# Kernel tuning notes

Measured on AMD Instinct MI355X. Metric: run time of the kernel, lower is better.

Reference implementation:

```python
import jax, jax.numpy as jnp
import numpy as np

B, T, N, F_IN, F_OUT = 2, 8, 8192, 128, 32

def setup_inputs() -> dict:
    key = jax.random.key(0)
    k1, k2, k3, k4 = jax.random.split(key, 4)
    inp = jax.random.normal(k1, (B, T, N, F_IN), dtype=jnp.float32)
    adj = jax.random.randint(k2, (N, N), 0, 2, dtype=jnp.int32)
    # xavier_uniform with gain=1.414 ~ std = gain*sqrt(2/(fan_in+fan_out)); gaussian approx
    w_std = 1.414 * np.sqrt(2.0 / (F_IN + F_OUT))
    a_std = 1.414 * np.sqrt(2.0 / (2 * F_OUT + N))
    W = jax.random.normal(k3, (F_IN, F_OUT), dtype=jnp.float32) * w_std
    a = jax.random.normal(k4, (2 * F_OUT, N), dtype=jnp.float32) * a_std
    return {"inp": inp, "adj": adj, "W": W, "a": a}

def reference(inp, adj, W, a):
    # h: [B,T,N,out]
    h = jnp.einsum('btni,io->btno', inp, W)
    out = W.shape[1]
    # mask[j,i] = 1 if j is a neighbor of i (original: torch.where(adj[:, i] > 0))
    mask = (adj > 0).astype(h.dtype)
    # neighbor sum per destination node i: [B,T,N,out]
    nbr = jnp.einsum('ji,btjo->btio', mask, h)
    a1 = a[:out].T   # [N, out], per-node first half of attention vector
    a2 = a[out:].T   # [N, out], per-node second half
    # scalar score per (b,t,i); broadcast across j in the original attention matrix.
    # no-neighbor case coincides since nbr is zero there.
    s = jnp.einsum('btno,no->btn', h, a1) + jnp.einsum('btno,no->btn', nbr, a2)
    # h_prime[b,t,i,:] = s[b,t,i] * sum_j h[b,t,j,:]  (attention row is constant)
    h_prime = s[..., None] * jnp.sum(h, axis=2, keepdims=True)
    return jax.nn.relu(h_prime)
```

## Files before the change

### kernel.cpp

```cpp
#include <hip/hip_runtime.h>

#define BT 16
#define NN 8192
#define FIN 128
#define FOUT 32
#define NB 512
#define SPLITK 4
#define KSPAN (NN / SPLITK)
#define BKK 32
#define NT 64
#define PADA 40

typedef __attribute__((ext_vector_type(8))) short short8;
typedef __attribute__((ext_vector_type(4))) float float4v;

__device__ __forceinline__ float bf2f(unsigned short u) {
    unsigned v = ((unsigned)u) << 16;
    float f;
    __builtin_memcpy(&f, &v, 4);
    return f;
}
__device__ __forceinline__ unsigned short f2bf(float f) {
    unsigned u;
    __builtin_memcpy(&u, &f, 4);
    u += 0x7FFFu + ((u >> 16) & 1u);
    return (unsigned short)(u >> 16);
}

__device__ __forceinline__ void load_lds16(const unsigned short* g, unsigned short* l) {
    __builtin_amdgcn_global_load_lds((const __attribute__((address_space(1))) void*)g,
                                     (__attribute__((address_space(3))) void*)l, 16, 0, 0);
}

__global__ void sniff_dtype(const unsigned* __restrict__ Wraw, unsigned* __restrict__ flag,
                            float* __restrict__ sumh) {
    int lane = threadIdx.x;
    unsigned u = Wraw[lane];
    float f = bf2f((unsigned short)(u & 0xFFFFu));
    float af = fabsf(f);
    bool plaus = (af > 1e-5f) && (af < 1e3f);
    unsigned long long msk = __ballot(plaus);
    if (lane == 0) flag[0] = (__popcll(msk) >= 32) ? 1u : 0u;
#pragma unroll
    for (int r = 0; r < 8; ++r) sumh[lane + 64 * r] = 0.f;
}

__launch_bounds__(256)
__global__ void k1(const void* __restrict__ inp_raw, const void* __restrict__ W_raw,
                   unsigned short* __restrict__ Ht, float* __restrict__ sumh,
                   float4* __restrict__ s2v, const unsigned* __restrict__ flagp) {
    __shared__ __align__(16) unsigned short Wt[32 * 136];
    int bid = blockIdx.x;
    const int tid = threadIdx.x;

    if (bid < 128) {
        float4 z; z.x = z.y = z.z = z.w = 0.f;
        s2v[bid * 256 + tid] = z;
        return;
    }
    bid -= 128;
    const int bt = bid >> 6;
    const int j0 = (bid & 63) * 128;
    const bool isbf = (*flagp != 0u);

    if (isbf) {
        const unsigned short* Wb = (const unsigned short*)W_raw;
#pragma unroll
        for (int r = 0; r < 16; ++r) {
            int idx = tid + 256 * r, i = idx >> 5, o = idx & 31;
            Wt[o * 136 + i] = Wb[idx];
        }
    } else {
        const float* Wf = (const float*)W_raw;
#pragma unroll
        for (int r = 0; r < 16; ++r) {
            int idx = tid + 256 * r, i = idx >> 5, o = idx & 31;
            Wt[o * 136 + i] = f2bf(Wf[idx]);
        }
    }
    __syncthreads();

    const int lane = tid & 63, w = tid >> 6;
    const int m = lane & 15, q = lane >> 4;
    const int mt = (w & 1) * 16;
    const int nt = (w >> 1) * 64;

    float4v acc[4];
#pragma unroll
    for (int c = 0; c < 4; ++c) { float4v z = {0.f, 0.f, 0.f, 0.f}; acc[c] = z; }

#pragma unroll
    for (int kstep = 0; kstep < 4; ++kstep) {
        short8 af = *(const short8*)&Wt[(mt + m) * 136 + kstep * 32 + q * 8];
#pragma unroll
        for (int c = 0; c < 4; ++c) {
            int j = j0 + nt + c * 16 + m;
            short8 bfrag;
            if (isbf) {
                bfrag = *(const short8*)((const unsigned short*)inp_raw +
                        ((size_t)bt * NN + j) * FIN + kstep * 32 + q * 8);
            } else {
                const float* fp = (const float*)inp_raw + ((size_t)bt * NN + j) * FIN + kstep * 32 + q * 8;
                float4 f0 = *(const float4*)fp;
                float4 f1 = *(const float4*)(fp + 4);
                union { unsigned short u[8]; short8 v; } t;
                t.u[0] = f2bf(f0.x); t.u[1] = f2bf(f0.y); t.u[2] = f2bf(f0.z); t.u[3] = f2bf(f0.w);
                t.u[4] = f2bf(f1.x); t.u[5] = f2bf(f1.y); t.u[6] = f2bf(f1.z); t.u[7] = f2bf(f1.w);
                bfrag = t.v;
            }
            acc[c] = __builtin_amdgcn_mfma_f32_16x16x32_bf16(af, bfrag, acc[c], 0, 0, 0);
        }
    }

#pragma unroll
    for (int c = 0; c < 4; ++c) {
#pragma unroll
        for (int e = 0; e < 4; ++e) {
            int o = mt + q * 4 + e;
            int j = j0 + nt + c * 16 + m;
            Ht[(size_t)(bt * FOUT + o) * NN + j] = f2bf(acc[c][e]);
        }
    }
#pragma unroll
    for (int e = 0; e < 4; ++e) {
        float s = acc[0][e] + acc[1][e] + acc[2][e] + acc[3][e];
        s += __shfl_xor(s, 1); s += __shfl_xor(s, 2);
        s += __shfl_xor(s, 4); s += __shfl_xor(s, 8);
        if (m == 0) atomicAdd(&sumh[bt * FOUT + mt + q * 4 + e], s);
    }
}

__launch_bounds__(512, 4)
__global__ void k2_fused(const int* __restrict__ adj, const unsigned short* __restrict__ Ht,
                         const void* __restrict__ a_raw, float* __restrict__ s2,
                         const unsigned* __restrict__ flagp) {
    __shared__ int Pl[KSPAN * 2];
    __shared__ __align__(16) unsigned short As[64 * PADA];
    __shared__ __align__(16) unsigned short Bs[512 * 32];
    const int tid = threadIdx.x;
    const int lane = tid & 63;
    const int w = tid >> 6;
    const int m = lane & 15, q = lane >> 4;
    const int wn = w * 64;

    const int bid = blockIdx.x;
    const int xcd = bid & 7;
    const int z = xcd >> 1;
    const int ib = (bid >> 3) | ((xcd & 1) << 6);
    const int i0 = ib * 64;
    const int zbase = z * KSPAN;

    {
        const int* arow = adj + (size_t)zbase * NN + i0 + lane;
        for (int r0 = 0; r0 < 256; r0 += 16) {
            int v[16];
#pragma unroll
            for (int j = 0; j < 16; ++j)
                v[j] = arow[(size_t)(w * 256 + r0 + j) * NN];
#pragma unroll
            for (int j = 0; j < 16; ++j) {
                unsigned long long b = __ballot(v[j] > 0);
                if (lane == 0) {
                    int k = w * 256 + r0 + j;
                    int2 t;
                    t.x = (int)(unsigned)(b & 0xFFFFFFFFull);
                    t.y = (int)(unsigned)(b >> 32);
                    *(int2*)&Pl[k * 2] = t;
                }
            }
        }
    }

    int boff[4];
#pragma unroll
    for (int c = 0; c < 4; ++c) {
        int u = (w * 4 + c) * 64 + lane;
        int kbs = (u & 3) ^ ((u >> 3) & 3);
        boff[c] = (u >> 2) * NN + kbs * 8;
    }

    float4v acc[4][4];
#pragma unroll
    for (int r = 0; r < 4; ++r)
#pragma unroll
        for (int c = 0; c < 4; ++c) { float4v zz = {0.f, 0.f, 0.f, 0.f}; acc[r][c] = zz; }

    __syncthreads();

    for (int t = 0; t < NT; ++t) {
#pragma unroll
        for (int c = 0; c < 4; ++c)
            load_lds16(Ht + boff[c] + zbase + t * BKK, &Bs[(w * 4 + c) * 512]);
        {
            const int kb = t * BKK + w * 4;
            const int h = lane >> 5, sh = lane & 31;
            unsigned w0 = ((unsigned)Pl[(kb + 0) * 2 + h] >> sh) & 1u;
            unsigned w1 = ((unsigned)Pl[(kb + 1) * 2 + h] >> sh) & 1u;
            unsigned w2 = ((unsigned)Pl[(kb + 2) * 2 + h] >> sh) & 1u;
            unsigned w3 = ((unsigned)Pl[(kb + 3) * 2 + h] >> sh) & 1u;
            int2 tt;
            tt.x = (int)((w0 ? 0x3F80u : 0u) | (w1 ? 0x3F800000u : 0u));
            tt.y = (int)((w2 ? 0x3F80u : 0u) | (w3 ? 0x3F800000u : 0u));
            *(int2*)&As[lane * PADA + w * 4] = tt;
        }
        __syncthreads();
        short8 af[4];
#pragma unroll
        for (int r = 0; r < 4; ++r)
            af[r] = *(const short8*)&As[(r * 16 + m) * PADA + q * 8];
#pragma unroll
        for (int c = 0; c < 4; ++c) {
            int row = wn + c * 16 + m;
            int kbs = q ^ ((m >> 1) & 3);
            short8 bfr = *(const short8*)&Bs[row * 32 + kbs * 8];
#pragma unroll
            for (int r = 0; r < 4; ++r)
                acc[r][c] = __builtin_amdgcn_mfma_f32_16x16x32_bf16(af[r], bfr, acc[r][c], 0, 0, 0);
        }
        __syncthreads();
    }

    const bool isbf = (*flagp != 0u);
    const int btA = wn >> 5;
#pragma unroll
    for (int r = 0; r < 4; ++r) {
#pragma unroll
        for (int e = 0; e < 4; ++e) {
            int gi = i0 + r * 16 + q * 4 + e;
            float a2m, a2m16;
            if (isbf) {
                const unsigned short* ab = (const unsigned short*)a_raw;
                a2m   = bf2f(ab[(size_t)(FOUT + m) * NN + gi]);
                a2m16 = bf2f(ab[(size_t)(FOUT + 16 + m) * NN + gi]);
            } else {
                const float* afp = (const float*)a_raw;
                a2m   = afp[(size_t)(FOUT + m) * NN + gi];
                a2m16 = afp[(size_t)(FOUT + 16 + m) * NN + gi];
            }
            float sA = acc[r][0][e] * a2m + acc[r][1][e] * a2m16;
            float sB = acc[r][2][e] * a2m + acc[r][3][e] * a2m16;
            sA += __shfl_xor(sA, 1); sA += __shfl_xor(sA, 2);
            sA += __shfl_xor(sA, 4); sA += __shfl_xor(sA, 8);
            sB += __shfl_xor(sB, 1); sB += __shfl_xor(sB, 2);
            sB += __shfl_xor(sB, 4); sB += __shfl_xor(sB, 8);
            if (m == 0) {
                atomicAdd(&s2[(size_t)btA * NN + gi], sA);
                atomicAdd(&s2[(size_t)(btA + 1) * NN + gi], sB);
            }
        }
    }
}

__launch_bounds__(256)
__global__ void k3_out(const unsigned short* __restrict__ Ht, const float* __restrict__ s2,
                       const float* __restrict__ sumh, const void* __restrict__ a_raw,
                       void* __restrict__ out_raw, const unsigned* __restrict__ flagp) {
    const int i = blockIdx.x * 256 + threadIdx.x;
    const int bt = blockIdx.y;
    const bool isbf = (*flagp != 0u);

    float s = s2[(size_t)bt * NN + i];
    if (isbf) {
        const unsigned short* ab = (const unsigned short*)a_raw;
#pragma unroll
        for (int o = 0; o < 32; ++o) {
            float h = bf2f(Ht[(size_t)(bt * FOUT + o) * NN + i]);
            s += h * bf2f(ab[(size_t)o * NN + i]);
        }
    } else {
        const float* afp = (const float*)a_raw;
#pragma unroll
        for (int o = 0; o < 32; ++o) {
            float h = bf2f(Ht[(size_t)(bt * FOUT + o) * NN + i]);
            s += h * afp[(size_t)o * NN + i];
        }
    }

    float ov[32];
#pragma unroll
    for (int o = 0; o < 32; ++o) ov[o] = fmaxf(s * sumh[bt * FOUT + o], 0.f);

    size_t ob = ((size_t)bt * NN + i) * FOUT;
    if (isbf) {
        unsigned short* o16 = (unsigned short*)out_raw + ob;
#pragma unroll
        for (int c = 0; c < 8; ++c) {
            ushort4 p;
            p.x = f2bf(ov[c * 4 + 0]); p.y = f2bf(ov[c * 4 + 1]);
            p.z = f2bf(ov[c * 4 + 2]); p.w = f2bf(ov[c * 4 + 3]);
            *(ushort4*)(o16 + c * 4) = p;
        }
    } else {
        float* of = (float*)out_raw + ob;
#pragma unroll
        for (int c = 0; c < 8; ++c) {
            float4 v;
            v.x = ov[c * 4 + 0]; v.y = ov[c * 4 + 1]; v.z = ov[c * 4 + 2]; v.w = ov[c * 4 + 3];
            *(float4*)(of + c * 4) = v;
        }
    }
}

extern "C" void kernel_launch(void* const* d_in, const int* in_sizes, int n_in,
                              void* d_out, int out_size, void* d_ws, size_t ws_size,
                              hipStream_t stream) {
    const void* inp = d_in[0];
    const int* adj = (const int*)d_in[1];
    const void* W = d_in[2];
    const void* a = d_in[3];

    char* ws = (char*)d_ws;
    unsigned short* Ht = (unsigned short*)ws;
    unsigned* flag = (unsigned*)(ws + 8388608);
    float* s2 = (float*)(ws + 8388608 + 4096);
    float* sumh = (float*)(ws + 8388608 + 4096 + 524288);

    sniff_dtype<<<1, 64, 0, stream>>>((const unsigned*)W, flag, sumh);
    k1<<<1152, 256, 0, stream>>>(inp, W, Ht, sumh, (float4*)s2, flag);
    k2_fused<<<512, 512, 0, stream>>>(adj, Ht, a, s2, flag);
    k3_out<<<dim3(NN / 256, BT), 256, 0, stream>>>(Ht, s2, sumh, a, d_out, flag);
}
```

Measured before the change: 539.6 us.

## Reassociate neighbor score as H·a2 then masked sum, row-major H layout

The neighbor-aggregation kernel now computes h_j·a2_i for every (j,i) pair with MFMA and then applies the adjacency mask as per-element FMAs. Before, it formed the masked matrix product mask^T·H and dotted the result with a2 afterwards. H is stored row-major ([bt,j,o]) so each node's features load as contiguous vectors in k1, k2 and k3. The k2 tiling changes to 512-wide i tiles, 256-long k spans and 1024-thread blocks that accumulate all 16 bt slices in registers. This removes the bf16 mask-matrix build in LDS and the large accumulator tile, in exchange for many small MFMAs with zero initial accumulators, masked scalar reduction work, and a2 converted to bf16.

```diff
diff --git a/kernel.cpp b/kernel.cpp
--- a/kernel.cpp
+++ b/kernel.cpp
@@ -4,12 +4,9 @@
 #define NN 8192
 #define FIN 128
 #define FOUT 32
-#define NB 512
-#define SPLITK 4
-#define KSPAN (NN / SPLITK)
-#define BKK 32
-#define NT 64
-#define PADA 40
+#define ITILE 512
+#define KSP 256
+#define NSTEP 16
 
 typedef __attribute__((ext_vector_type(8))) short short8;
 typedef __attribute__((ext_vector_type(4))) float float4v;
@@ -47,7 +44,7 @@
 
 __launch_bounds__(256)
 __global__ void k1(const void* __restrict__ inp_raw, const void* __restrict__ W_raw,
-                   unsigned short* __restrict__ Ht, float* __restrict__ sumh,
+                   unsigned short* __restrict__ H, float* __restrict__ sumh,
                    float4* __restrict__ s2v, const unsigned* __restrict__ flagp) {
     __shared__ __align__(16) unsigned short Wt[32 * 136];
     int bid = blockIdx.x;
@@ -114,12 +111,11 @@
 
 #pragma unroll
     for (int c = 0; c < 4; ++c) {
-#pragma unroll
-        for (int e = 0; e < 4; ++e) {
-            int o = mt + q * 4 + e;
-            int j = j0 + nt + c * 16 + m;
-            Ht[(size_t)(bt * FOUT + o) * NN + j] = f2bf(acc[c][e]);
-        }
+        int j = j0 + nt + c * 16 + m;
+        ushort4 p;
+        p.x = f2bf(acc[c][0]); p.y = f2bf(acc[c][1]);
+        p.z = f2bf(acc[c][2]); p.w = f2bf(acc[c][3]);
+        *(ushort4*)&H[((size_t)bt * NN + j) * FOUT + mt + q * 4] = p;
     }
 #pragma unroll
     for (int e = 0; e < 4; ++e) {
@@ -130,129 +126,115 @@
     }
 }
 
-__launch_bounds__(512, 4)
-__global__ void k2_fused(const int* __restrict__ adj, const unsigned short* __restrict__ Ht,
+__launch_bounds__(1024, 8)
+__global__ void k2_fused(const int* __restrict__ adj, const unsigned short* __restrict__ H,
                          const void* __restrict__ a_raw, float* __restrict__ s2,
                          const unsigned* __restrict__ flagp) {
-    __shared__ int Pl[KSPAN * 2];
-    __shared__ __align__(16) unsigned short As[64 * PADA];
-    __shared__ __align__(16) unsigned short Bs[512 * 32];
+    __shared__ int Pl[KSP * 16];
+    __shared__ __align__(16) unsigned short Hs[16 * 512];
     const int tid = threadIdx.x;
     const int lane = tid & 63;
     const int w = tid >> 6;
     const int m = lane & 15, q = lane >> 4;
-    const int wn = w * 64;
 
     const int bid = blockIdx.x;
-    const int xcd = bid & 7;
-    const int z = xcd >> 1;
-    const int ib = (bid >> 3) | ((xcd & 1) << 6);
-    const int i0 = ib * 64;
-    const int zbase = z * KSPAN;
+    const int ib = bid & 15;
+    const int z = bid >> 4;
+    const int i0 = ib * ITILE;
+    const int k0 = z * KSP;
 
     {
-        const int* arow = adj + (size_t)zbase * NN + i0 + lane;
-        for (int r0 = 0; r0 < 256; r0 += 16) {
+        const size_t kb = (size_t)(k0 + w * 16);
+        for (int lr = 0; lr < 16; lr += 2) {
             int v[16];
 #pragma unroll
-            for (int j = 0; j < 16; ++j)
-                v[j] = arow[(size_t)(w * 256 + r0 + j) * NN];
+            for (int j = 0; j < 16; ++j) {
+                int row = lr + (j >> 3), c = j & 7;
+                v[j] = adj[(kb + row) * NN + i0 + c * 64 + lane];
+            }
 #pragma unroll
             for (int j = 0; j < 16; ++j) {
                 unsigned long long b = __ballot(v[j] > 0);
                 if (lane == 0) {
-                    int k = w * 256 + r0 + j;
+                    int row = w * 16 + lr + (j >> 3), c = j & 7;
                     int2 t;
                     t.x = (int)(unsigned)(b & 0xFFFFFFFFull);
                     t.y = (int)(unsigned)(b >> 32);
-                    *(int2*)&Pl[k * 2] = t;
+                    *(int2*)&Pl[row * 16 + c * 2] = t;
                 }
             }
         }
     }
 
-    int boff[4];
-#pragma unroll
-    for (int c = 0; c < 4; ++c) {
-        int u = (w * 4 + c) * 64 + lane;
-        int kbs = (u & 3) ^ ((u >> 3) & 3);
-        boff[c] = (u >> 2) * NN + kbs * 8;
-    }
-
-    float4v acc[4][4];
-#pragma unroll
-    for (int r = 0; r < 4; ++r)
-#pragma unroll
-        for (int c = 0; c < 4; ++c) { float4v zz = {0.f, 0.f, 0.f, 0.f}; acc[r][c] = zz; }
+    const bool isbf = (*flagp != 0u);
+    short8 a2f[2];
+#pragma unroll
+    for (int s = 0; s < 2; ++s) {
+        int gi = i0 + (w * 2 + s) * 16 + m;
+        union { unsigned short u[8]; short8 v; } t;
+        if (isbf) {
+            const unsigned short* ab = (const unsigned short*)a_raw;
+#pragma unroll
+            for (int tt = 0; tt < 8; ++tt)
+                t.u[tt] = ab[(size_t)(FOUT + q * 8 + tt) * NN + gi];
+        } else {
+            const float* afp = (const float*)a_raw;
+#pragma unroll
+            for (int tt = 0; tt < 8; ++tt)
+                t.u[tt] = f2bf(afp[(size_t)(FOUT + q * 8 + tt) * NN + gi]);
+        }
+        a2f[s] = t.v;
+    }
+
+    const int soff = ((lane >> 2) * 32) + (((lane & 3) ^ ((lane >> 4) & 3)) * 8);
+    const int rsl = (m * 4 + (q ^ ((m >> 2) & 3))) * 8;
+
+    float s2acc[16][2];
+#pragma unroll
+    for (int bt = 0; bt < 16; ++bt) { s2acc[bt][0] = 0.f; s2acc[bt][1] = 0.f; }
 
     __syncthreads();
 
-    for (int t = 0; t < NT; ++t) {
-#pragma unroll
-        for (int c = 0; c < 4; ++c)
-            load_lds16(Ht + boff[c] + zbase + t * BKK, &Bs[(w * 4 + c) * 512]);
-        {
-            const int kb = t * BKK + w * 4;
-            const int h = lane >> 5, sh = lane & 31;
-            unsigned w0 = ((unsigned)Pl[(kb + 0) * 2 + h] >> sh) & 1u;
-            unsigned w1 = ((unsigned)Pl[(kb + 1) * 2 + h] >> sh) & 1u;
-            unsigned w2 = ((unsigned)Pl[(kb + 2) * 2 + h] >> sh) & 1u;
-            unsigned w3 = ((unsigned)Pl[(kb + 3) * 2 + h] >> sh) & 1u;
-            int2 tt;
-            tt.x = (int)((w0 ? 0x3F80u : 0u) | (w1 ? 0x3F800000u : 0u));
-            tt.y = (int)((w2 ? 0x3F80u : 0u) | (w3 ? 0x3F800000u : 0u));
-            *(int2*)&As[lane * PADA + w * 4] = tt;
+    for (int st = 0; st < NSTEP; ++st) {
+        load_lds16(H + ((size_t)w * NN + k0 + st * 16) * 32 + soff, &Hs[w * 512]);
+        float mskf[2][4];
+#pragma unroll
+        for (int e = 0; e < 4; ++e) {
+            unsigned wrd = (unsigned)Pl[(st * 16 + q * 4 + e) * 16 + w];
+            mskf[0][e] = ((wrd >> m) & 1u) ? 1.f : 0.f;
+            mskf[1][e] = ((wrd >> (16 + m)) & 1u) ? 1.f : 0.f;
         }
         __syncthreads();
-        short8 af[4];
-#pragma unroll
-        for (int r = 0; r < 4; ++r)
-            af[r] = *(const short8*)&As[(r * 16 + m) * PADA + q * 8];
-#pragma unroll
-        for (int c = 0; c < 4; ++c) {
-            int row = wn + c * 16 + m;
-            int kbs = q ^ ((m >> 1) & 3);
-            short8 bfr = *(const short8*)&Bs[row * 32 + kbs * 8];
-#pragma unroll
-            for (int r = 0; r < 4; ++r)
-                acc[r][c] = __builtin_amdgcn_mfma_f32_16x16x32_bf16(af[r], bfr, acc[r][c], 0, 0, 0);
+#pragma unroll
+        for (int bt = 0; bt < 16; ++bt) {
+            short8 af = *(const short8*)&Hs[bt * 512 + rsl];
+#pragma unroll
+            for (int s = 0; s < 2; ++s) {
+                float4v D = {0.f, 0.f, 0.f, 0.f};
+                D = __builtin_amdgcn_mfma_f32_16x16x32_bf16(af, a2f[s], D, 0, 0, 0);
+#pragma unroll
+                for (int e = 0; e < 4; ++e)
+                    s2acc[bt][s] = fmaf(mskf[s][e], D[e], s2acc[bt][s]);
+            }
         }
         __syncthreads();
     }
 
-    const bool isbf = (*flagp != 0u);
-    const int btA = wn >> 5;
-#pragma unroll
-    for (int r = 0; r < 4; ++r) {
-#pragma unroll
-        for (int e = 0; e < 4; ++e) {
-            int gi = i0 + r * 16 + q * 4 + e;
-            float a2m, a2m16;
-            if (isbf) {
-                const unsigned short* ab = (const unsigned short*)a_raw;
-                a2m   = bf2f(ab[(size_t)(FOUT + m) * NN + gi]);
-                a2m16 = bf2f(ab[(size_t)(FOUT + 16 + m) * NN + gi]);
-            } else {
-                const float* afp = (const float*)a_raw;
-                a2m   = afp[(size_t)(FOUT + m) * NN + gi];
-                a2m16 = afp[(size_t)(FOUT + 16 + m) * NN + gi];
-            }
-            float sA = acc[r][0][e] * a2m + acc[r][1][e] * a2m16;
-            float sB = acc[r][2][e] * a2m + acc[r][3][e] * a2m16;
-            sA += __shfl_xor(sA, 1); sA += __shfl_xor(sA, 2);
-            sA += __shfl_xor(sA, 4); sA += __shfl_xor(sA, 8);
-            sB += __shfl_xor(sB, 1); sB += __shfl_xor(sB, 2);
-            sB += __shfl_xor(sB, 4); sB += __shfl_xor(sB, 8);
-            if (m == 0) {
-                atomicAdd(&s2[(size_t)btA * NN + gi], sA);
-                atomicAdd(&s2[(size_t)(btA + 1) * NN + gi], sB);
-            }
+#pragma unroll
+    for (int bt = 0; bt < 16; ++bt) {
+#pragma unroll
+        for (int s = 0; s < 2; ++s) {
+            float v = s2acc[bt][s];
+            v += __shfl_xor(v, 16);
+            v += __shfl_xor(v, 32);
+            if (q == 0)
+                atomicAdd(&s2[(size_t)bt * NN + i0 + (w * 2 + s) * 16 + m], v);
         }
     }
 }
 
 __launch_bounds__(256)
-__global__ void k3_out(const unsigned short* __restrict__ Ht, const float* __restrict__ s2,
+__global__ void k3_out(const unsigned short* __restrict__ H, const float* __restrict__ s2,
                        const float* __restrict__ sumh, const void* __restrict__ a_raw,
                        void* __restrict__ out_raw, const unsigned* __restrict__ flagp) {
     const int i = blockIdx.x * 256 + threadIdx.x;
@@ -260,19 +242,28 @@
     const bool isbf = (*flagp != 0u);
 
     float s = s2[(size_t)bt * NN + i];
+    const unsigned short* hp = H + ((size_t)bt * NN + i) * FOUT;
     if (isbf) {
         const unsigned short* ab = (const unsigned short*)a_raw;
 #pragma unroll
-        for (int o = 0; o < 32; ++o) {
-            float h = bf2f(Ht[(size_t)(bt * FOUT + o) * NN + i]);
-            s += h * bf2f(ab[(size_t)o * NN + i]);
+        for (int ob = 0; ob < 4; ++ob) {
+            short8 hv = *(const short8*)(hp + ob * 8);
+#pragma unroll
+            for (int t = 0; t < 8; ++t) {
+                int o = ob * 8 + t;
+                s += bf2f((unsigned short)hv[t]) * bf2f(ab[(size_t)o * NN + i]);
+            }
         }
     } else {
         const float* afp = (const float*)a_raw;
 #pragma unroll
-        for (int o = 0; o < 32; ++o) {
-            float h = bf2f(Ht[(size_t)(bt * FOUT + o) * NN + i]);
-            s += h * afp[(size_t)o * NN + i];
+        for (int ob = 0; ob < 4; ++ob) {
+            short8 hv = *(const short8*)(hp + ob * 8);
+#pragma unroll
+            for (int t = 0; t < 8; ++t) {
+                int o = ob * 8 + t;
+                s += bf2f((unsigned short)hv[t]) * afp[(size_t)o * NN + i];
+            }
         }
     }
 
@@ -280,9 +271,9 @@
 #pragma unroll
     for (int o = 0; o < 32; ++o) ov[o] = fmaxf(s * sumh[bt * FOUT + o], 0.f);
 
-    size_t ob = ((size_t)bt * NN + i) * FOUT;
+    size_t ob2 = ((size_t)bt * NN + i) * FOUT;
     if (isbf) {
-        unsigned short* o16 = (unsigned short*)out_raw + ob;
+        unsigned short* o16 = (unsigned short*)out_raw + ob2;
 #pragma unroll
         for (int c = 0; c < 8; ++c) {
             ushort4 p;
@@ -291,7 +282,7 @@
             *(ushort4*)(o16 + c * 4) = p;
         }
     } else {
-        float* of = (float*)out_raw + ob;
+        float* of = (float*)out_raw + ob2;
 #pragma unroll
         for (int c = 0; c < 8; ++c) {
             float4 v;
@@ -310,13 +301,13 @@
     const void* a = d_in[3];
 
     char* ws = (char*)d_ws;
-    unsigned short* Ht = (unsigned short*)ws;
+    unsigned short* H = (unsigned short*)ws;
     unsigned* flag = (unsigned*)(ws + 8388608);
     float* s2 = (float*)(ws + 8388608 + 4096);
     float* sumh = (float*)(ws + 8388608 + 4096 + 524288);
 
     sniff_dtype<<<1, 64, 0, stream>>>((const unsigned*)W, flag, sumh);
-    k1<<<1152, 256, 0, stream>>>(inp, W, Ht, sumh, (float4*)s2, flag);
-    k2_fused<<<512, 512, 0, stream>>>(adj, Ht, a, s2, flag);
-    k3_out<<<dim3(NN / 256, BT), 256, 0, stream>>>(Ht, s2, sumh, a, d_out, flag);
-}
+    k1<<<1152, 256, 0, stream>>>(inp, W, H, sumh, (float4*)s2, flag);
+    k2_fused<<<512, 1024, 0, stream>>>(adj, H, a, s2, flag);
+    k3_out<<<dim3(NN / 256, BT), 256, 0, stream>>>(H, s2, sumh, a, d_out, flag);
+}
```

After: 1.450 ms. 169% more time.
